# Optimization experiments

Hardware: AMD Instinct MI355X
Metric: run time of the kernel (lower is better)

Reference implementation:

```python
import jax, jax.numpy as jnp
import numpy as np

EARTH_RADIUS = 6371000.0
OMEGA = 7.292e-05
F0 = 1e-4
N_SQUARED = 1e-4
TARGET_SLOPE = -3.0


def _fd(x, h, axis):
    """torch.gradient equivalent: 2nd-order central interior, 1st-order one-sided edges."""
    n = x.shape[axis]
    def sl(a, b):
        idx = [slice(None)] * x.ndim
        idx[axis] = slice(a, b)
        return x[tuple(idx)]
    interior = (sl(2, n) - sl(0, n - 2)) / (2.0 * h)
    first = (sl(1, 2) - sl(0, 1)) / h
    last = (sl(n - 1, n) - sl(n - 2, n - 1)) / h
    return jnp.concatenate([first, interior, last], axis=axis)


def setup_inputs() -> dict:
    key = jax.random.key(0)
    k1, k2 = jax.random.split(key)
    B, L, LAT, LON = 2, 13, 721, 1440
    u = 10.0 * jax.random.normal(k1, (B, L, LAT, LON), dtype=jnp.float32)
    v = 10.0 * jax.random.normal(k2, (B, L, LAT, LON), dtype=jnp.float32)
    pressure_levels = jnp.linspace(50.0, 1000.0, L).astype(jnp.float32)
    return {"u": u, "v": v, "pressure_levels": pressure_levels}


def _losses(u, v, pressure_levels):
    B, L, LAT, LON = u.shape
    lat = jnp.linspace(-np.pi / 2, np.pi / 2, LAT, dtype=u.dtype)
    dlat = np.pi / (LAT - 1)
    dlon = 2 * np.pi / LON
    cos_lat = jnp.clip(jnp.cos(lat), 1e-8, None).reshape(1, 1, LAT, 1)
    dx = EARTH_RADIUS * cos_lat  # [1,1,LAT,1]
    dy = EARTH_RADIUS

    # ---- PV conservation loss ----
    dvdx = _fd(v, dlon, 3) / dx
    dudy = _fd(u, dlat, 2) / dy
    vorticity = dvdx - dudy
    f = (2.0 * OMEGA * jnp.sin(lat)).reshape(1, 1, LAT, 1)
    abs_vorticity = vorticity + f
    dp = jnp.mean(jnp.diff(pressure_levels)) * 100.0  # hPa -> Pa
    vort_p = _fd(vorticity, dp, 1)
    vort_pp = _fd(vort_p, dp, 1)
    qg_pv = abs_vorticity + (F0 ** 2 / N_SQUARED) * vort_pp
    pv_variance = jnp.var(qg_pv, axis=(-2, -1), ddof=1).mean()  # torch.var is unbiased
    pv_grad_lat = _fd(qg_pv, dlat, 2) / dy
    pv_grad_lon = _fd(qg_pv, dlon, 3) / dx
    pv_loss = pv_variance + 0.1 * jnp.mean(pv_grad_lat ** 2 + pv_grad_lon ** 2)

    # ---- Energy spectra loss (radial FFT binning) ----
    ke_mean = (0.5 * (u ** 2 + v ** 2)).mean(axis=(0, 1))  # [LAT,LON]
    power_spectrum = jnp.abs(jnp.fft.rfft2(ke_mean, norm='ortho')) ** 2
    fy = np.fft.fftfreq(LAT, d=1.0)
    fx = np.fft.rfftfreq(LON, d=1.0)
    k_radial = np.sqrt(fy[:, None] ** 2 + fx[None, :] ** 2)
    k_max = min(LAT, LON) // 4
    k_bins = np.linspace(1.0, float(k_max), 20)
    # static (shape-only) binning: digitize into 19 bins, out-of-range -> bin 19
    bidx = np.digitize(k_radial.ravel(), k_bins) - 1
    bidx = np.where((bidx < 0) | (bidx > 18), 19, bidx)
    counts = np.bincount(bidx, minlength=20)[:19]
    valid = counts > 0
    if int(valid.sum()) >= 3:
        sums = jax.ops.segment_sum(power_spectrum.ravel(), jnp.asarray(bidx), num_segments=20)[:19]
        spectrum = sums[valid] / jnp.asarray(counts[valid], dtype=power_spectrum.dtype)
        centers = ((k_bins[:-1] + k_bins[1:]) / 2.0)[valid]
        log_k = jnp.log(jnp.asarray(centers, dtype=u.dtype) + 1e-8)
        log_s = jnp.log(spectrum + 1e-8)
        lkm = log_k.mean()
        lsm = log_s.mean()
        slope = ((log_k - lkm) * (log_s - lsm)).sum() / (((log_k - lkm) ** 2).sum() + 1e-8)
        spectra_loss = (slope - TARGET_SLOPE) ** 2
    else:
        # Note: with d=1.0 fftfreq (max |k| ~ 0.707 < k_bins[0]=1) all bins are
        # empty, so the original torch code returns 0.0 here as well.
        spectra_loss = jnp.asarray(0.0, dtype=u.dtype)

    # ---- Mass-weighted column divergence loss ----
    dudx = _fd(u, dlon, 3) / dx
    dvdy = _fd(v, dlat, 2) / dy
    divergence = dudx + dvdy
    p = pressure_levels * 100.0
    dpl = jnp.diff(p)  # [L-1]
    w = jnp.concatenate([dpl[:1] / 2, (dpl[:-1] + dpl[1:]) / 2, dpl[-1:] / 2])  # trapezoid
    w = (w / jnp.clip(w.sum(), 1e-8, None)).reshape(1, L, 1, 1)
    column_div = (divergence * w).sum(axis=1)
    mass_loss = jnp.mean(column_div ** 2)

    return pv_loss + spectra_loss + mass_loss


def reference(u, v, pressure_levels):
    return _losses(u, v, pressure_levels)
```

## Files before the change

kernel.cpp:

```cpp
#include <hip/hip_runtime.h>
#include <math.h>

#define LATN 721
#define LONN 1440
#define NLEV 13
#define NBATCH 2
#define SLICE (LATN * LONN)
#define BATSTRIDE (NLEV * SLICE)

#define OUTW 60
#define WGCOLS 240
#define SEGS 6
#define NROWP 361
#define NWGX (NROWP * SEGS)

#define NBANK      128
#define BANKSTRIDE 64
#define WS_ACC     0
#define ACC_SUM    0
#define ACC_SSQ    26
#define ACC_GRAD   28
#define ACC_MASS   29
#define N_ACC      30
#define WS_INVDX   (NBANK * BANKSTRIDE)
#define WS_FCOR    (WS_INVDX + LATN)
#define WS_W       (WS_FCOR + LATN)
#define WS_INVDP   (WS_W + NLEV)
#define WS_INV2DP  (WS_INVDP + 1)

constexpr float INV_R     = (float)(1.0 / 6371000.0);
constexpr float INV_DLAT  = (float)(720.0 / M_PI);
constexpr float INV_2DLAT = (float)(360.0 / M_PI);
constexpr float INV_DLON  = (float)(1440.0 / (2.0 * M_PI));
constexpr float INV_2DLON = (float)(720.0 / (2.0 * M_PI));
constexpr float QG_COEF   = 1e-4f;

__global__ void pl_setup_kernel(const float* __restrict__ plev, float* __restrict__ ws) {
    const int t = threadIdx.x;
    if (t < LATN) {
        double lat;
        if (t == 0)            lat = (double)(-(float)(M_PI / 2.0));
        else if (t == LATN-1)  lat = (double)( (float)(M_PI / 2.0));
        else                   lat = (double)((float)(-M_PI / 2.0 + (double)t * (M_PI / 720.0)));
        double c = cos(lat);
        if (c < 1e-8) c = 1e-8;
        ws[WS_INVDX + t] = (float)(1.0 / (6371000.0 * c));
        ws[WS_FCOR  + t] = (float)(2.0 * 7.292e-05 * sin(lat));
    }
    if (t < NLEV) {
        float p[NLEV];
        #pragma unroll
        for (int l = 0; l < NLEV; ++l) p[l] = plev[l] * 100.0f;
        float dpl[NLEV-1];
        #pragma unroll
        for (int l = 0; l < NLEV-1; ++l) dpl[l] = p[l+1] - p[l];
        float raw;
        if (t == 0)            raw = dpl[0] * 0.5f;
        else if (t == NLEV-1)  raw = dpl[NLEV-2] * 0.5f;
        else                   raw = (dpl[t-1] + dpl[t]) * 0.5f;
        float s = dpl[0] * 0.5f + dpl[NLEV-2] * 0.5f;
        #pragma unroll
        for (int l = 1; l < NLEV-1; ++l) s += (dpl[l-1] + dpl[l]) * 0.5f;
        if (s < 1e-8f) s = 1e-8f;
        ws[WS_W + t] = raw / s;
    }
    if (t == 0) {
        float sd = 0.f;
        for (int l = 0; l < NLEV-1; ++l) sd += plev[l+1] - plev[l];
        float dp = sd / (float)(NLEV-1) * 100.0f;
        ws[WS_INVDP]  = 1.0f / dp;
        ws[WS_INV2DP] = 1.0f / (2.0f * dp);
    }
    for (int z = t; z < NBANK * BANKSTRIDE; z += 1024) ws[WS_ACC + z] = 0.0f;
}

__device__ __forceinline__ int swz_nwg(int orig, int nwg) {
    const int q = nwg >> 3, r = nwg & 7;
    const int x = orig & 7, k = orig >> 3;
    return (x < r ? x * (q + 1) : r * (q + 1) + (x - r) * q) + k;
}

__launch_bounds__(256)
__global__ void pl_row2m_kernel(const float* __restrict__ u, const float* __restrict__ v,
                                float* __restrict__ ws)
{
    __shared__ float red[16][17];

    const int tid  = threadIdx.x;
    const int lane = tid & 63, w = tid >> 6;
    const int b  = blockIdx.y;
    const int wg = swz_nwg(blockIdx.x, NWGX);
    const int wgr = wg / SEGS, seg = wg - wgr * SEGS;
    const int r0  = 2 * wgr;

    const int out0 = seg * WGCOLS + w * OUTW;
    const int c_un = out0 - 2 + lane;
    const int c = max(0, min(c_un, LONN - 1));
    const float ma = (lane >= 2 && lane <= 61) ? 1.f : 0.f;
    const float mb = (r0 + 1 < LATN) ? ma : 0.f;
    const bool e0 = (c == 0), e1 = (c == LONN - 1);
    const bool rTop = (r0 == 0), rBotA = (r0 == LATN - 1);

    const int crm = max(r0 - 1, 0);
    const int crb = min(r0 + 1, LATN - 1);
    const int crp = min(r0 + 2, LATN - 1);
    const int cu0 = max(r0 - 2, 0), cu1 = crm, cu2 = r0;
    const int cu3 = crb, cu4 = crp, cu5 = min(r0 + 3, LATN - 1);

    const float* ub = u + (size_t)b * BATSTRIDE;
    const float* vb = v + (size_t)b * BATSTRIDE;
    const float idp = ws[WS_INVDP], i2dp = ws[WS_INV2DP];

    const float eC = (e0 || e1) ? INV_DLON : INV_2DLON;
    const float sc_m = eC * ws[WS_INVDX + crm];
    const float sc_a = eC * ws[WS_INVDX + r0];
    const float sc_b = eC * ws[WS_INVDX + crb];
    const float sc_p = eC * ws[WS_INVDX + crp];
    const float sr_a = ((rTop || rBotA) ? INV_DLAT : INV_2DLAT) * INV_R;
    const float sr_mb = INV_2DLAT * INV_R;
    const float sr_p = ((r0 + 2 >= LATN - 1) ? INV_DLAT : INV_2DLAT) * INV_R;
    const float fc_m = ws[WS_FCOR + crm], fc_a = ws[WS_FCOR + r0];
    const float fc_b = ws[WS_FCOR + crb], fc_p = ws[WS_FCOR + crp];

    const int o_u0 = cu0 * LONN + c, o_u1 = cu1 * LONN + c, o_u2 = cu2 * LONN + c;
    const int o_u3 = cu3 * LONN + c, o_u4 = cu4 * LONN + c, o_u5 = cu5 * LONN + c;
    const int o_vm = crm * LONN + c, o_va = r0 * LONN + c;
    const int o_vb = crb * LONN + c, o_vp = crp * LONN + c;

    float vals[16];
    #pragma unroll
    for (int k = 0; k < 16; ++k) vals[k] = 0.f;
    float ssqt = 0.f, grad = 0.f;
    float wu_a = 0.f, wu_b = 0.f, wvm = 0.f, wva = 0.f, wvb = 0.f, wvp = 0.f;

    auto consume = [&](int k, float qm, float qa, float qb, float qp) {
        const float qx = qa * ma, qy = qb * mb;
        vals[k] += qx + qy;
        ssqt += qx * qx + qy * qy;
        const float gla = (qb - qm) * sr_a;
        const float glb = (qp - qa) * sr_mb;
        const float qaL = __shfl_up(qa, 1), qaR = __shfl_down(qa, 1);
        const float qbL = __shfl_up(qb, 1), qbR = __shfl_down(qb, 1);
        const float gna = ((e1 ? qa : qaR) - (e0 ? qa : qaL)) * sc_a;
        const float gnb = ((e1 ? qb : qbR) - (e0 ? qb : qbL)) * sc_b;
        grad += ma * (gla * gla + gna * gna) + mb * (glb * glb + gnb * gnb);
    };

    float vo2_m, vo1_m, pa_m, pb_m;
    float vo2_a, vo1_a, pa_a, pb_a;
    float vo2_b, vo1_b, pa_b, pb_b;
    float vo2_p, vo1_p, pa_p, pb_p;

    const float* pu = ub;
    const float* pv = vb;
    #pragma unroll
    for (int l = 0; l < NLEV; ++l) {
        const float wl = ws[WS_W + l];
        const float u0 = pu[o_u0], u1 = pu[o_u1], u2 = pu[o_u2];
        const float u3 = pu[o_u3], u4 = pu[o_u4], u5 = pu[o_u5];
        const float vm = pv[o_vm], va = pv[o_va], vbv = pv[o_vb], vpp = pv[o_vp];

        const float vmL = __shfl_up(vm, 1),  vmR = __shfl_down(vm, 1);
        const float vaL = __shfl_up(va, 1),  vaR = __shfl_down(va, 1);
        const float vbL = __shfl_up(vbv, 1), vbR = __shfl_down(vbv, 1);
        const float vpL = __shfl_up(vpp, 1), vpR = __shfl_down(vpp, 1);

        float com = (vmR - vmL) * sc_m - (u2 - u0) * sr_mb;
        float coa = (vaR - vaL) * sc_a - (u3 - u1) * sr_a;
        float cob = (vbR - vbL) * sc_b - (u4 - u2) * sr_mb;
        float cop = (vpR - vpL) * sc_p - (u5 - u3) * sr_p;
        if (rTop)  com = coa;
        if (rBotA) { cob = coa; cop = coa; }

        wu_a = fmaf(wl, u2, wu_a);   wu_b = fmaf(wl, u3, wu_b);
        wvm = fmaf(wl, vm, wvm);     wva = fmaf(wl, va, wva);
        wvb = fmaf(wl, vbv, wvb);    wvp = fmaf(wl, vpp, wvp);

        if (l == 0) {
            vo1_m = com; vo1_a = coa; vo1_b = cob; vo1_p = cop;
        } else if (l == 1) {
            pb_m = (com - vo1_m) * idp;  pb_a = (coa - vo1_a) * idp;
            pb_b = (cob - vo1_b) * idp;  pb_p = (cop - vo1_p) * idp;
            vo2_m = vo1_m; vo1_m = com;  vo2_a = vo1_a; vo1_a = coa;
            vo2_b = vo1_b; vo1_b = cob;  vo2_p = vo1_p; vo1_p = cop;
        } else {
            const float pn_m = (com - vo2_m) * i2dp;
            const float pn_a = (coa - vo2_a) * i2dp;
            const float pn_b = (cob - vo2_b) * i2dp;
            const float pn_p = (cop - vo2_p) * i2dp;
            float qm, qa, qb, qp;
            if (l == 2) {
                qm = vo2_m + fc_m + QG_COEF * ((pn_m - pb_m) * idp);
                qa = vo2_a + fc_a + QG_COEF * ((pn_a - pb_a) * idp);
                qb = vo2_b + fc_b + QG_COEF * ((pn_b - pb_b) * idp);
                qp = vo2_p + fc_p + QG_COEF * ((pn_p - pb_p) * idp);
            } else {
                qm = vo2_m + fc_m + QG_COEF * ((pn_m - pa_m) * i2dp);
                qa = vo2_a + fc_a + QG_COEF * ((pn_a - pa_a) * i2dp);
                qb = vo2_b + fc_b + QG_COEF * ((pn_b - pa_b) * i2dp);
                qp = vo2_p + fc_p + QG_COEF * ((pn_p - pa_p) * i2dp);
            }
            consume(l - 2, qm, qa, qb, qp);
            pa_m = pb_m; pb_m = pn_m;  vo2_m = vo1_m; vo1_m = com;
            pa_a = pb_a; pb_a = pn_a;  vo2_a = vo1_a; vo1_a = coa;
            pa_b = pb_b; pb_b = pn_b;  vo2_b = vo1_b; vo1_b = cob;
            pa_p = pb_p; pb_p = pn_p;  vo2_p = vo1_p; vo1_p = cop;
        }
        pu += SLICE; pv += SLICE;
    }
    {
        const float p12m = (vo1_m - vo2_m) * idp;
        const float p12a = (vo1_a - vo2_a) * idp;
        const float p12b = (vo1_b - vo2_b) * idp;
        const float p12p = (vo1_p - vo2_p) * idp;
        consume(11, vo2_m + fc_m + QG_COEF * ((p12m - pa_m) * i2dp),
                    vo2_a + fc_a + QG_COEF * ((p12a - pa_a) * i2dp),
                    vo2_b + fc_b + QG_COEF * ((p12b - pa_b) * i2dp),
                    vo2_p + fc_p + QG_COEF * ((p12p - pa_p) * i2dp));
        consume(12, vo1_m + fc_m + QG_COEF * ((p12m - pb_m) * idp),
                    vo1_a + fc_a + QG_COEF * ((p12a - pb_a) * idp),
                    vo1_b + fc_b + QG_COEF * ((p12b - pb_b) * idp),
                    vo1_p + fc_p + QG_COEF * ((p12p - pb_p) * idp));
    }

    vals[13] += ssqt;
    vals[14] += grad;
    {
        const float waL = __shfl_up(wu_a, 1), waR = __shfl_down(wu_a, 1);
        const float wbL = __shfl_up(wu_b, 1), wbR = __shfl_down(wu_b, 1);
        const float cda = ((e1 ? wu_a : waR) - (e0 ? wu_a : waL)) * sc_a + (wvb - wvm) * sr_a;
        const float cdb = ((e1 ? wu_b : wbR) - (e0 ? wu_b : wbL)) * sc_b + (wvp - wva) * sr_mb;
        vals[15] += ma * cda * cda + mb * cdb * cdb;
    }

    #pragma unroll
    for (int k = 0; k < 16; ++k) {
        float x = vals[k];
        x += __shfl_xor(x, 8, 64);
        x += __shfl_xor(x, 4, 64);
        x += __shfl_xor(x, 2, 64);
        x += __shfl_xor(x, 1, 64);
        vals[k] = x;
    }
    const int g = tid >> 4, k16 = tid & 15;
    float myv = vals[0];
    #pragma unroll
    for (int k = 1; k < 16; ++k) if (k16 == k) myv = vals[k];
    red[g][k16] = myv;
    __syncthreads();

    if (tid < 16) {
        const int k = tid;
        float s = 0.f;
        #pragma unroll
        for (int g2 = 0; g2 < 16; ++g2) s += red[g2][k];
        int target;
        if (k < 13)       target = ACC_SUM + b * 13 + k;
        else if (k == 13) target = ACC_SSQ + b;
        else if (k == 14) target = ACC_GRAD;
        else              target = ACC_MASS;
        const int bank = (b * NWGX + blockIdx.x) & (NBANK - 1);
        atomicAdd(&ws[WS_ACC + bank * BANKSTRIDE + target], s);
    }
}

__global__ void pl_finalize_kernel(const float* __restrict__ ws, float* __restrict__ out) {
    __shared__ float tot[N_ACC];
    const int t = threadIdx.x;
    if (t < N_ACC) {
        float s = 0.f;
        for (int bk = 0; bk < NBANK; ++bk) s += ws[WS_ACC + bk * BANKSTRIDE + t];
        tot[t] = s;
    }
    __syncthreads();
    if (t == 0) {
        const float N = (float)SLICE;
        float s2 = 0.f;
        for (int s = 0; s < 2 * NLEV; ++s) s2 += tot[ACC_SUM + s] * tot[ACC_SUM + s];
        const float ssq = tot[ACC_SSQ + 0] + tot[ACC_SSQ + 1];
        float vmean = (ssq - s2 / N) / (N - 1.0f) * (1.0f / (2.0f * NLEV));
        float gmean = tot[ACC_GRAD] / (float)(NBATCH * NLEV * SLICE);
        float mmean = tot[ACC_MASS] / (float)(NBATCH * SLICE);
        out[0] = vmean + 0.1f * gmean + mmean;
    }
}

extern "C" void kernel_launch(void* const* d_in, const int* in_sizes, int n_in,
                              void* d_out, int out_size, void* d_ws, size_t ws_size,
                              hipStream_t stream) {
    const float* u    = (const float*)d_in[0];
    const float* v    = (const float*)d_in[1];
    const float* plev = (const float*)d_in[2];
    float* ws  = (float*)d_ws;
    float* out = (float*)d_out;

    hipLaunchKernelGGL(pl_setup_kernel, dim3(1), dim3(1024), 0, stream, plev, ws);
    hipLaunchKernelGGL(pl_row2m_kernel, dim3(NWGX, NBATCH), dim3(256), 0, stream, u, v, ws);
    hipLaunchKernelGGL(pl_finalize_kernel, dim3(1), dim3(64), 0, stream, ws, out);
}
```

Baseline: 67.93 us.

## Process two columns per lane with float2 loads to cut halo overhead

Each lane now handles two adjacent longitude columns through float2 vector loads, and the per-wave output width grows from 60 to 124 columns, which halves the number of column segments per row pair. The aim is to shrink the share of redundant halo lanes, halve the wave-shuffle and load-instruction count per output point, and widen memory transactions. In exchange each thread holds more registers, which could lower occupancy, and the grid has fewer workgroups. The edge masks and the handling at the longitude boundaries also become more intricate.

```diff
diff --git a/kernel.cpp b/kernel.cpp
--- a/kernel.cpp
+++ b/kernel.cpp
@@ -8,9 +8,9 @@
 #define SLICE (LATN * LONN)
 #define BATSTRIDE (NLEV * SLICE)
 
-#define OUTW 60
-#define WGCOLS 240
-#define SEGS 6
+#define OUTW 124
+#define WGCOLS 496
+#define SEGS 3
 #define NROWP 361
 #define NWGX (NROWP * SEGS)
 
@@ -79,10 +79,16 @@
     const int x = orig & 7, k = orig >> 3;
     return (x < r ? x * (q + 1) : r * (q + 1) + (x - r) * q) + k;
 }
+__device__ __forceinline__ float2 ld2(const float* p) {
+    return *reinterpret_cast<const float2*>(p);
+}
+__device__ __forceinline__ float2 sm2(float2 a, float2 b, float s) {
+    return make_float2((a.x - b.x) * s, (a.y - b.y) * s);
+}
 
 __launch_bounds__(256)
-__global__ void pl_row2m_kernel(const float* __restrict__ u, const float* __restrict__ v,
-                                float* __restrict__ ws)
+__global__ void pl_rc22_kernel(const float* __restrict__ u, const float* __restrict__ v,
+                               float* __restrict__ ws)
 {
     __shared__ float red[16][17];
 
@@ -93,14 +99,17 @@
     const int wgr = wg / SEGS, seg = wg - wgr * SEGS;
     const int r0  = 2 * wgr;
 
-    const int out0 = seg * WGCOLS + w * OUTW;
-    const int c_un = out0 - 2 + lane;
-    const int c = max(0, min(c_un, LONN - 1));
-    const float ma = (lane >= 2 && lane <= 61) ? 1.f : 0.f;
-    const float mb = (r0 + 1 < LATN) ? ma : 0.f;
-    const bool e0 = (c == 0), e1 = (c == LONN - 1);
+    const int out0  = seg * WGCOLS + w * OUTW;
+    const int c0_un = out0 - 2 + 2 * lane;
+    const int cb = max(0, min(c0_un, LONN - 2));
+    const float m0 = (lane >= 1 && lane <= 62 && c0_un     < LONN) ? 1.f : 0.f;
+    const float m1 = (lane >= 1 && lane <= 62 && c0_un + 1 < LONN) ? 1.f : 0.f;
+    const bool e0 = (c0_un == 0);
+    const bool e1 = (c0_un + 1 == LONN - 1);
+
     const bool rTop = (r0 == 0), rBotA = (r0 == LATN - 1);
-
+    const float rbf = (r0 + 1 < LATN) ? 1.f : 0.f;
+    const float mb0 = m0 * rbf, mb1 = m1 * rbf;
     const int crm = max(r0 - 1, 0);
     const int crb = min(r0 + 1, LATN - 1);
     const int crp = min(r0 + 2, LATN - 1);
@@ -111,94 +120,115 @@
     const float* vb = v + (size_t)b * BATSTRIDE;
     const float idp = ws[WS_INVDP], i2dp = ws[WS_INV2DP];
 
-    const float eC = (e0 || e1) ? INV_DLON : INV_2DLON;
-    const float sc_m = eC * ws[WS_INVDX + crm];
-    const float sc_a = eC * ws[WS_INVDX + r0];
-    const float sc_b = eC * ws[WS_INVDX + crb];
-    const float sc_p = eC * ws[WS_INVDX + crp];
+    const float eC0 = e0 ? INV_DLON : INV_2DLON;
+    const float eC1 = e1 ? INV_DLON : INV_2DLON;
+    const float ixm = ws[WS_INVDX + crm], ixa = ws[WS_INVDX + r0];
+    const float ixb = ws[WS_INVDX + crb], ixp = ws[WS_INVDX + crp];
+    const float sm0 = eC0 * ixm, sm1 = eC1 * ixm;
+    const float sa0 = eC0 * ixa, sa1 = eC1 * ixa;
+    const float sb0 = eC0 * ixb, sb1 = eC1 * ixb;
+    const float sp0 = eC0 * ixp, sp1 = eC1 * ixp;
     const float sr_a = ((rTop || rBotA) ? INV_DLAT : INV_2DLAT) * INV_R;
     const float sr_mb = INV_2DLAT * INV_R;
     const float sr_p = ((r0 + 2 >= LATN - 1) ? INV_DLAT : INV_2DLAT) * INV_R;
     const float fc_m = ws[WS_FCOR + crm], fc_a = ws[WS_FCOR + r0];
     const float fc_b = ws[WS_FCOR + crb], fc_p = ws[WS_FCOR + crp];
 
-    const int o_u0 = cu0 * LONN + c, o_u1 = cu1 * LONN + c, o_u2 = cu2 * LONN + c;
-    const int o_u3 = cu3 * LONN + c, o_u4 = cu4 * LONN + c, o_u5 = cu5 * LONN + c;
-    const int o_vm = crm * LONN + c, o_va = r0 * LONN + c;
-    const int o_vb = crb * LONN + c, o_vp = crp * LONN + c;
+    const int o_u0 = cu0 * LONN + cb, o_u1 = cu1 * LONN + cb, o_u2 = cu2 * LONN + cb;
+    const int o_u3 = cu3 * LONN + cb, o_u4 = cu4 * LONN + cb, o_u5 = cu5 * LONN + cb;
+    const int o_vm = crm * LONN + cb, o_va = r0 * LONN + cb;
+    const int o_vb = crb * LONN + cb, o_vp = crp * LONN + cb;
 
     float vals[16];
     #pragma unroll
     for (int k = 0; k < 16; ++k) vals[k] = 0.f;
     float ssqt = 0.f, grad = 0.f;
-    float wu_a = 0.f, wu_b = 0.f, wvm = 0.f, wva = 0.f, wvb = 0.f, wvp = 0.f;
-
-    auto consume = [&](int k, float qm, float qa, float qb, float qp) {
-        const float qx = qa * ma, qy = qb * mb;
-        vals[k] += qx + qy;
-        ssqt += qx * qx + qy * qy;
-        const float gla = (qb - qm) * sr_a;
-        const float glb = (qp - qa) * sr_mb;
-        const float qaL = __shfl_up(qa, 1), qaR = __shfl_down(qa, 1);
-        const float qbL = __shfl_up(qb, 1), qbR = __shfl_down(qb, 1);
-        const float gna = ((e1 ? qa : qaR) - (e0 ? qa : qaL)) * sc_a;
-        const float gnb = ((e1 ? qb : qbR) - (e0 ? qb : qbL)) * sc_b;
-        grad += ma * (gla * gla + gna * gna) + mb * (glb * glb + gnb * gnb);
+    float2 wu_a = make_float2(0.f, 0.f), wu_b = make_float2(0.f, 0.f);
+    float2 wvm = make_float2(0.f, 0.f), wva = make_float2(0.f, 0.f);
+    float2 wvb = make_float2(0.f, 0.f), wvp = make_float2(0.f, 0.f);
+
+    auto qgf = [&](float2 vo, float fc, float2 vpp) -> float2 {
+        return make_float2(vo.x + fc + QG_COEF * vpp.x, vo.y + fc + QG_COEF * vpp.y);
     };
-
-    float vo2_m, vo1_m, pa_m, pb_m;
-    float vo2_a, vo1_a, pa_a, pb_a;
-    float vo2_b, vo1_b, pa_b, pb_b;
-    float vo2_p, vo1_p, pa_p, pb_p;
+    auto consume = [&](int k, float2 qm, float2 qa, float2 qb, float2 qp) {
+        const float qax = qa.x * m0,  qay = qa.y * m1;
+        const float qbx = qb.x * mb0, qby = qb.y * mb1;
+        vals[k] += (qax + qay) + (qbx + qby);
+        ssqt += qax * qax + qay * qay + qbx * qbx + qby * qby;
+        const float2 gla = sm2(qb, qm, sr_a);
+        const float2 glb = sm2(qp, qa, sr_mb);
+        const float qaL = __shfl_up(qa.y, 1), qaR = __shfl_down(qa.x, 1);
+        const float qbL = __shfl_up(qb.y, 1), qbR = __shfl_down(qb.x, 1);
+        const float gnax = (qa.y - (e0 ? qa.x : qaL)) * sa0;
+        const float gnay = ((e1 ? qa.y : qaR) - qa.x) * sa1;
+        const float gnbx = (qb.y - (e0 ? qb.x : qbL)) * sb0;
+        const float gnby = ((e1 ? qb.y : qbR) - qb.x) * sb1;
+        grad += m0  * (gla.x * gla.x + gnax * gnax) + m1  * (gla.y * gla.y + gnay * gnay)
+              + mb0 * (glb.x * glb.x + gnbx * gnbx) + mb1 * (glb.y * glb.y + gnby * gnby);
+    };
+
+    float2 vo2_m, vo1_m, pa_m, pb_m;
+    float2 vo2_a, vo1_a, pa_a, pb_a;
+    float2 vo2_b, vo1_b, pa_b, pb_b;
+    float2 vo2_p, vo1_p, pa_p, pb_p;
 
     const float* pu = ub;
     const float* pv = vb;
     #pragma unroll
     for (int l = 0; l < NLEV; ++l) {
         const float wl = ws[WS_W + l];
-        const float u0 = pu[o_u0], u1 = pu[o_u1], u2 = pu[o_u2];
-        const float u3 = pu[o_u3], u4 = pu[o_u4], u5 = pu[o_u5];
-        const float vm = pv[o_vm], va = pv[o_va], vbv = pv[o_vb], vpp = pv[o_vp];
-
-        const float vmL = __shfl_up(vm, 1),  vmR = __shfl_down(vm, 1);
-        const float vaL = __shfl_up(va, 1),  vaR = __shfl_down(va, 1);
-        const float vbL = __shfl_up(vbv, 1), vbR = __shfl_down(vbv, 1);
-        const float vpL = __shfl_up(vpp, 1), vpR = __shfl_down(vpp, 1);
-
-        float com = (vmR - vmL) * sc_m - (u2 - u0) * sr_mb;
-        float coa = (vaR - vaL) * sc_a - (u3 - u1) * sr_a;
-        float cob = (vbR - vbL) * sc_b - (u4 - u2) * sr_mb;
-        float cop = (vpR - vpL) * sc_p - (u5 - u3) * sr_p;
+        const float2 u0 = ld2(pu + o_u0), u1 = ld2(pu + o_u1), u2 = ld2(pu + o_u2);
+        const float2 u3 = ld2(pu + o_u3), u4 = ld2(pu + o_u4), u5 = ld2(pu + o_u5);
+        const float2 vm = ld2(pv + o_vm), va = ld2(pv + o_va);
+        const float2 vbv = ld2(pv + o_vb), vpv = ld2(pv + o_vp);
+
+        const float vmL = __shfl_up(vm.y, 1),  vmR = __shfl_down(vm.x, 1);
+        const float vaL = __shfl_up(va.y, 1),  vaR = __shfl_down(va.x, 1);
+        const float vbL = __shfl_up(vbv.y, 1), vbR = __shfl_down(vbv.x, 1);
+        const float vpL = __shfl_up(vpv.y, 1), vpR = __shfl_down(vpv.x, 1);
+
+        float2 com, coa, cob, cop;
+        com.x = (vm.y - (e0 ? vm.x : vmL)) * sm0 - (u2.x - u0.x) * sr_mb;
+        com.y = ((e1 ? vm.y : vmR) - vm.x) * sm1 - (u2.y - u0.y) * sr_mb;
+        coa.x = (va.y - (e0 ? va.x : vaL)) * sa0 - (u3.x - u1.x) * sr_a;
+        coa.y = ((e1 ? va.y : vaR) - va.x) * sa1 - (u3.y - u1.y) * sr_a;
+        cob.x = (vbv.y - (e0 ? vbv.x : vbL)) * sb0 - (u4.x - u2.x) * sr_mb;
+        cob.y = ((e1 ? vbv.y : vbR) - vbv.x) * sb1 - (u4.y - u2.y) * sr_mb;
+        cop.x = (vpv.y - (e0 ? vpv.x : vpL)) * sp0 - (u5.x - u3.x) * sr_p;
+        cop.y = ((e1 ? vpv.y : vpR) - vpv.x) * sp1 - (u5.y - u3.y) * sr_p;
         if (rTop)  com = coa;
         if (rBotA) { cob = coa; cop = coa; }
 
-        wu_a = fmaf(wl, u2, wu_a);   wu_b = fmaf(wl, u3, wu_b);
-        wvm = fmaf(wl, vm, wvm);     wva = fmaf(wl, va, wva);
-        wvb = fmaf(wl, vbv, wvb);    wvp = fmaf(wl, vpp, wvp);
+        wu_a.x = fmaf(wl, u2.x, wu_a.x);  wu_a.y = fmaf(wl, u2.y, wu_a.y);
+        wu_b.x = fmaf(wl, u3.x, wu_b.x);  wu_b.y = fmaf(wl, u3.y, wu_b.y);
+        wvm.x = fmaf(wl, vm.x, wvm.x);    wvm.y = fmaf(wl, vm.y, wvm.y);
+        wva.x = fmaf(wl, va.x, wva.x);    wva.y = fmaf(wl, va.y, wva.y);
+        wvb.x = fmaf(wl, vbv.x, wvb.x);   wvb.y = fmaf(wl, vbv.y, wvb.y);
+        wvp.x = fmaf(wl, vpv.x, wvp.x);   wvp.y = fmaf(wl, vpv.y, wvp.y);
 
         if (l == 0) {
             vo1_m = com; vo1_a = coa; vo1_b = cob; vo1_p = cop;
         } else if (l == 1) {
-            pb_m = (com - vo1_m) * idp;  pb_a = (coa - vo1_a) * idp;
-            pb_b = (cob - vo1_b) * idp;  pb_p = (cop - vo1_p) * idp;
-            vo2_m = vo1_m; vo1_m = com;  vo2_a = vo1_a; vo1_a = coa;
-            vo2_b = vo1_b; vo1_b = cob;  vo2_p = vo1_p; vo1_p = cop;
+            pb_m = sm2(com, vo1_m, idp);  pb_a = sm2(coa, vo1_a, idp);
+            pb_b = sm2(cob, vo1_b, idp);  pb_p = sm2(cop, vo1_p, idp);
+            vo2_m = vo1_m; vo1_m = com;   vo2_a = vo1_a; vo1_a = coa;
+            vo2_b = vo1_b; vo1_b = cob;   vo2_p = vo1_p; vo1_p = cop;
         } else {
-            const float pn_m = (com - vo2_m) * i2dp;
-            const float pn_a = (coa - vo2_a) * i2dp;
-            const float pn_b = (cob - vo2_b) * i2dp;
-            const float pn_p = (cop - vo2_p) * i2dp;
-            float qm, qa, qb, qp;
+            const float2 pn_m = sm2(com, vo2_m, i2dp);
+            const float2 pn_a = sm2(coa, vo2_a, i2dp);
+            const float2 pn_b = sm2(cob, vo2_b, i2dp);
+            const float2 pn_p = sm2(cop, vo2_p, i2dp);
+            float2 qm, qa, qb, qp;
             if (l == 2) {
-                qm = vo2_m + fc_m + QG_COEF * ((pn_m - pb_m) * idp);
-                qa = vo2_a + fc_a + QG_COEF * ((pn_a - pb_a) * idp);
-                qb = vo2_b + fc_b + QG_COEF * ((pn_b - pb_b) * idp);
-                qp = vo2_p + fc_p + QG_COEF * ((pn_p - pb_p) * idp);
+                qm = qgf(vo2_m, fc_m, sm2(pn_m, pb_m, idp));
+                qa = qgf(vo2_a, fc_a, sm2(pn_a, pb_a, idp));
+                qb = qgf(vo2_b, fc_b, sm2(pn_b, pb_b, idp));
+                qp = qgf(vo2_p, fc_p, sm2(pn_p, pb_p, idp));
             } else {
-                qm = vo2_m + fc_m + QG_COEF * ((pn_m - pa_m) * i2dp);
-                qa = vo2_a + fc_a + QG_COEF * ((pn_a - pa_a) * i2dp);
-                qb = vo2_b + fc_b + QG_COEF * ((pn_b - pa_b) * i2dp);
-                qp = vo2_p + fc_p + QG_COEF * ((pn_p - pa_p) * i2dp);
+                qm = qgf(vo2_m, fc_m, sm2(pn_m, pa_m, i2dp));
+                qa = qgf(vo2_a, fc_a, sm2(pn_a, pa_a, i2dp));
+                qb = qgf(vo2_b, fc_b, sm2(pn_b, pa_b, i2dp));
+                qp = qgf(vo2_p, fc_p, sm2(pn_p, pa_p, i2dp));
             }
             consume(l - 2, qm, qa, qb, qp);
             pa_m = pb_m; pb_m = pn_m;  vo2_m = vo1_m; vo1_m = com;
@@ -209,28 +239,31 @@
         pu += SLICE; pv += SLICE;
     }
     {
-        const float p12m = (vo1_m - vo2_m) * idp;
-        const float p12a = (vo1_a - vo2_a) * idp;
-        const float p12b = (vo1_b - vo2_b) * idp;
-        const float p12p = (vo1_p - vo2_p) * idp;
-        consume(11, vo2_m + fc_m + QG_COEF * ((p12m - pa_m) * i2dp),
-                    vo2_a + fc_a + QG_COEF * ((p12a - pa_a) * i2dp),
-                    vo2_b + fc_b + QG_COEF * ((p12b - pa_b) * i2dp),
-                    vo2_p + fc_p + QG_COEF * ((p12p - pa_p) * i2dp));
-        consume(12, vo1_m + fc_m + QG_COEF * ((p12m - pb_m) * idp),
-                    vo1_a + fc_a + QG_COEF * ((p12a - pb_a) * idp),
-                    vo1_b + fc_b + QG_COEF * ((p12b - pb_b) * idp),
-                    vo1_p + fc_p + QG_COEF * ((p12p - pb_p) * idp));
+        const float2 p12m = sm2(vo1_m, vo2_m, idp);
+        const float2 p12a = sm2(vo1_a, vo2_a, idp);
+        const float2 p12b = sm2(vo1_b, vo2_b, idp);
+        const float2 p12p = sm2(vo1_p, vo2_p, idp);
+        consume(11, qgf(vo2_m, fc_m, sm2(p12m, pa_m, i2dp)),
+                    qgf(vo2_a, fc_a, sm2(p12a, pa_a, i2dp)),
+                    qgf(vo2_b, fc_b, sm2(p12b, pa_b, i2dp)),
+                    qgf(vo2_p, fc_p, sm2(p12p, pa_p, i2dp)));
+        consume(12, qgf(vo1_m, fc_m, sm2(p12m, pb_m, idp)),
+                    qgf(vo1_a, fc_a, sm2(p12a, pb_a, idp)),
+                    qgf(vo1_b, fc_b, sm2(p12b, pb_b, idp)),
+                    qgf(vo1_p, fc_p, sm2(p12p, pb_p, idp)));
     }
 
     vals[13] += ssqt;
     vals[14] += grad;
     {
-        const float waL = __shfl_up(wu_a, 1), waR = __shfl_down(wu_a, 1);
-        const float wbL = __shfl_up(wu_b, 1), wbR = __shfl_down(wu_b, 1);
-        const float cda = ((e1 ? wu_a : waR) - (e0 ? wu_a : waL)) * sc_a + (wvb - wvm) * sr_a;
-        const float cdb = ((e1 ? wu_b : wbR) - (e0 ? wu_b : wbL)) * sc_b + (wvp - wva) * sr_mb;
-        vals[15] += ma * cda * cda + mb * cdb * cdb;
+        const float waL = __shfl_up(wu_a.y, 1), waR = __shfl_down(wu_a.x, 1);
+        const float wbL = __shfl_up(wu_b.y, 1), wbR = __shfl_down(wu_b.x, 1);
+        const float cdax = (wu_a.y - (e0 ? wu_a.x : waL)) * sa0 + (wvb.x - wvm.x) * sr_a;
+        const float cday = ((e1 ? wu_a.y : waR) - wu_a.x) * sa1 + (wvb.y - wvm.y) * sr_a;
+        const float cdbx = (wu_b.y - (e0 ? wu_b.x : wbL)) * sb0 + (wvp.x - wva.x) * sr_mb;
+        const float cdby = ((e1 ? wu_b.y : wbR) - wu_b.x) * sb1 + (wvp.y - wva.y) * sr_mb;
+        vals[15] += m0 * cdax * cdax + m1 * cday * cday
+                  + mb0 * cdbx * cdbx + mb1 * cdby * cdby;
     }
 
     #pragma unroll
@@ -295,6 +328,6 @@
     float* out = (float*)d_out;
 
     hipLaunchKernelGGL(pl_setup_kernel, dim3(1), dim3(1024), 0, stream, plev, ws);
-    hipLaunchKernelGGL(pl_row2m_kernel, dim3(NWGX, NBATCH), dim3(256), 0, stream, u, v, ws);
+    hipLaunchKernelGGL(pl_rc22_kernel, dim3(NWGX, NBATCH), dim3(256), 0, stream, u, v, ws);
     hipLaunchKernelGGL(pl_finalize_kernel, dim3(1), dim3(64), 0, stream, ws, out);
 }
```

Result: faster. 56.93 us (-16.2%).
